# Kernel tuning notes

Measured on AMD Instinct MI355X. Metric: run time of the kernel, lower is better.

The kernel has to match this reference:

```python
import jax, jax.numpy as jnp
import numpy as np

B, S, D, T = 64, 128, 512, 64  # batch, encoder len, dim_model, longest_coor

def setup_inputs() -> dict:
    key = jax.random.key(0)
    ks = jax.random.split(key, 10)
    def rn(k, shape, s=0.02):
        return jax.random.normal(k, shape, dtype=jnp.float32) * s
    return dict(
        e_all=jax.random.normal(ks[0], (B, S, D), dtype=jnp.float32),
        e_last=jax.random.normal(ks[1], (1, B, D), dtype=jnp.float32),
        Wa_w=rn(ks[2], (D, D)), Wa_b=jnp.zeros((D,), jnp.float32),
        Ua_w=rn(ks[3], (D, D)), Ua_b=jnp.zeros((D,), jnp.float32),
        Va_w=rn(ks[4], (D, 1)), Va_b=jnp.zeros((1,), jnp.float32),
        W_ih=rn(ks[5], (3 * D, D + 3)),  # GRU input weights, input = cat(attn[D], coord[3])
        W_hh=rn(ks[6], (3 * D, D)),
        b_ih=jnp.zeros((3 * D,), jnp.float32),
        b_hh=jnp.zeros((3 * D,), jnp.float32),
        Wo_w=rn(ks[7], (D, 3)), Wo_b=jnp.zeros((3,), jnp.float32),
    )

def reference(e_all, e_last, Wa_w, Wa_b, Ua_w, Ua_b, Va_w, Va_b,
              W_ih, W_hh, b_ih, b_hh, Wo_w, Wo_b):
    # Ua(keys) is step-invariant: hoist out of the decode loop (same math).
    Uk = e_all @ Ua_w + Ua_b                      # [B,S,D]
    h0 = e_last[0]                                # [B,D]
    x0 = jnp.zeros((e_all.shape[0], 3), e_all.dtype)

    def step(carry, _):
        h, x = carry
        # Bahdanau attention: query = current hidden state
        q = h @ Wa_w + Wa_b                       # [B,D]
        scores = jnp.squeeze(jnp.tanh(q[:, None, :] + Uk) @ Va_w, -1) + Va_b  # [B,S]
        w = jax.nn.softmax(scores, axis=-1)       # [B,S]
        ctx = jnp.einsum('bs,bsd->bd', w, e_all)  # [B,D]
        # single-step GRU, input = cat(context, prev coord)
        gin = jnp.concatenate([ctx, x], axis=-1)  # [B,D+3]
        gi = gin @ W_ih.T + b_ih                  # [B,3D]
        gh = h @ W_hh.T + b_hh                    # [B,3D]
        gir, giz, gin_n = jnp.split(gi, 3, axis=-1)
        ghr, ghz, ghn = jnp.split(gh, 3, axis=-1)
        r = jax.nn.sigmoid(gir + ghr)
        z = jax.nn.sigmoid(giz + ghz)
        n = jnp.tanh(gin_n + r * ghn)
        h_new = (1.0 - z) * n + z * h             # [B,D]
        out = h_new @ Wo_w + Wo_b                 # [B,3]
        return (h_new, out), (out, w)

    (hT, _), (outs, attns) = jax.lax.scan(step, (h0, x0), None, length=T)
    d_outputs = jnp.transpose(outs, (1, 0, 2))    # [B,T,3]
    cross_attn = jnp.transpose(attns, (1, 0, 2))  # [B,T,S]
    return d_outputs, hT[None], cross_attn
```

## Files before the change

### kernel.cpp

```cpp
#include <hip/hip_runtime.h>

typedef unsigned int u32;
typedef unsigned long long u64;
typedef float f32x4 __attribute__((ext_vector_type(4)));
typedef short short8 __attribute__((ext_vector_type(8)));

#define OFF_UKB 0u
#define OFF_QX  16777216u
#define OFF_EX  17563648u
#define G_BYTES 73728u

#define OFF_OUT_HT  12288u
#define OFF_OUT_ATT 45056u

#define NBLK 192
#define NTHR 512
#define DYN_LDS 145408
#define PREP_LDS 36864

__device__ __forceinline__ float fast_rcp(float x) { return __builtin_amdgcn_rcpf(x); }
__device__ __forceinline__ float tanh5(float x) {
    float e = __expf(2.f * x);
    return 1.f - 2.f * fast_rcp(e + 1.f);
}
__device__ __forceinline__ float sigm_f(float x) { return fast_rcp(1.f + __expf(-x)); }

__device__ __forceinline__ u32 packbf2(float a, float b) {
    u32 ua = __float_as_uint(a); ua += 0x7FFFu + ((ua >> 16) & 1u);
    u32 ub = __float_as_uint(b); ub += 0x7FFFu + ((ub >> 16) & 1u);
    return (ua >> 16) | (ub & 0xFFFF0000u);
}
__device__ __forceinline__ float2 unpackbf2(u32 u) {
    return make_float2(__uint_as_float(u << 16), __uint_as_float(u & 0xFFFF0000u));
}
__device__ __forceinline__ float bf16hi(float x, float& lo) {
    u32 u = __float_as_uint(x); u += 0x7FFFu + ((u >> 16) & 1u); u &= 0xFFFF0000u;
    const float h = __uint_as_float(u); lo = x - h; return h;
}

__device__ __forceinline__ u64 cload64(const u64* p) {
    return __hip_atomic_load(p, __ATOMIC_RELAXED, __HIP_MEMORY_SCOPE_AGENT);
}
__device__ __forceinline__ void cstore64(u64* p, u64 v) {
    __hip_atomic_store(p, v, __ATOMIC_RELAXED, __HIP_MEMORY_SCOPE_AGENT);
}
__device__ __forceinline__ u32 cload32(const u32* p) {
    return __hip_atomic_load(p, __ATOMIC_RELAXED, __HIP_MEMORY_SCOPE_AGENT);
}
__device__ __forceinline__ void cstore32(u32* p, u32 v) {
    __hip_atomic_store(p, v, __ATOMIC_RELAXED, __HIP_MEMORY_SCOPE_AGENT);
}

union U8 { u32 u[4]; uint4 q; short8 s; };

__global__ __launch_bounds__(256) void prep_kernel(
    const float* __restrict__ e_all, const float* __restrict__ e_last,
    const float* __restrict__ Ua_w,  const float* __restrict__ Ua_b,
    float* __restrict__ ws)
{
    extern __shared__ char pls[];
    u32* Ahi = (u32*)pls;
    u32* Alo = Ahi + 64 * 36;
    u32* Bhi = Alo + 64 * 36;
    u32* Blo = Bhi + 64 * 36;

    u32* UKB = (u32*)((char*)ws + OFF_UKB);

    const int blk = blockIdx.x, tid = threadIdx.x;
    const int gtid = blk * 256 + tid, gstride = 1024 * 256;

    for (int i = gtid; i < 5120; i += gstride) {
        const int g = i / 1280, j = i - g * 1280;
        ((u32*)((char*)ws + OFF_EX + (size_t)g * G_BYTES + 65536))[j] = 0u;
    }
    for (int i = gtid; i < 65536; i += gstride)
        ((u64*)((char*)ws + OFF_QX))[i] = 0ull;
    for (int i = gtid; i < 8192; i += gstride) {
        const int g = i >> 11, i2 = i & 2047;
        const float* ep = e_last + ((size_t)(g * 16 + (i2 >> 7)) * 512) + 4 * (i2 & 127);
        u64* HX = (u64*)((char*)ws + OFF_EX + (size_t)g * G_BYTES);
        HX[i2] = (u64)packbf2(ep[0], ep[1]) | ((u64)packbf2(ep[2], ep[3]) << 32);
    }

    const int r0 = (blk >> 3) * 64, c0 = (blk & 7) * 64;
    const int lane = tid & 63, wv = tid >> 6;
    const int mn = lane & 15, quad = lane >> 4;

    f32x4 acc[4];
    #pragma unroll
    for (int rg = 0; rg < 4; ++rg) acc[rg] = (f32x4){0.f, 0.f, 0.f, 0.f};

    for (int ks = 0; ks < 8; ++ks) {
        if (ks) __syncthreads();
        for (int i = tid; i < 1024; i += 256) {
            const int row = i >> 4, q4i = i & 15;
            const float4 e = *(const float4*)(e_all + (size_t)(r0 + row) * 512 + ks * 64 + 4 * q4i);
            float l0, l1, l2, l3;
            const float h0 = bf16hi(e.x, l0), h1 = bf16hi(e.y, l1);
            const float h2 = bf16hi(e.z, l2), h3 = bf16hi(e.w, l3);
            Ahi[row * 36 + 2 * q4i]     = packbf2(h0, h1);
            Ahi[row * 36 + 2 * q4i + 1] = packbf2(h2, h3);
            Alo[row * 36 + 2 * q4i]     = packbf2(l0, l1);
            Alo[row * 36 + 2 * q4i + 1] = packbf2(l2, l3);
        }
        for (int i = tid; i < 2048; i += 256) {
            const int col = i & 63, kp = i >> 6;
            const float b0 = Ua_w[(size_t)(ks * 64 + 2 * kp) * 512 + c0 + col];
            const float b1 = Ua_w[(size_t)(ks * 64 + 2 * kp + 1) * 512 + c0 + col];
            float l0, l1;
            const float h0 = bf16hi(b0, l0), h1 = bf16hi(b1, l1);
            Bhi[col * 36 + kp] = packbf2(h0, h1);
            Blo[col * 36 + kp] = packbf2(l0, l1);
        }
        __syncthreads();
        #pragma unroll
        for (int kb = 0; kb < 2; ++kb) {
            const int fo = kb * 16 + quad * 4;
            U8 bh, bl;
            bh.q = *(const uint4*)(Bhi + (wv * 16 + mn) * 36 + fo);
            bl.q = *(const uint4*)(Blo + (wv * 16 + mn) * 36 + fo);
            #pragma unroll
            for (int rg = 0; rg < 4; ++rg) {
                U8 ah, al;
                ah.q = *(const uint4*)(Ahi + (rg * 16 + mn) * 36 + fo);
                al.q = *(const uint4*)(Alo + (rg * 16 + mn) * 36 + fo);
                acc[rg] = __builtin_amdgcn_mfma_f32_16x16x32_bf16(al.s, bh.s, acc[rg], 0, 0, 0);
                acc[rg] = __builtin_amdgcn_mfma_f32_16x16x32_bf16(ah.s, bl.s, acc[rg], 0, 0, 0);
                acc[rg] = __builtin_amdgcn_mfma_f32_16x16x32_bf16(ah.s, bh.s, acc[rg], 0, 0, 0);
            }
        }
    }
    const int col = c0 + wv * 16 + mn;
    const float bias = Ua_b[col];
    #pragma unroll
    for (int rg = 0; rg < 4; ++rg) {
        #pragma unroll
        for (int reg = 0; reg < 4; ++reg) {
            const float v = acc[rg][reg] + bias;
            const float v1 = __shfl_down(v, 1);
            if (!(mn & 1))
                UKB[(size_t)(r0 + rg * 16 + quad * 4 + reg) * 256 + (col >> 1)] = packbf2(v, v1);
        }
    }
}

__global__ __launch_bounds__(512, 1) void decode_kernel(
    const float* __restrict__ e_all,
    const float* __restrict__ e_last,
    const float* __restrict__ Wa_w,  const float* __restrict__ Wa_b,
    const float* __restrict__ Va_w,
    const float* __restrict__ W_ih,  const float* __restrict__ W_hh,
    const float* __restrict__ b_ih,  const float* __restrict__ b_hh,
    const float* __restrict__ Wo_w,  const float* __restrict__ Wo_b,
    float* __restrict__ out, float* __restrict__ ws)
{
    extern __shared__ char smraw[];

    const u32* UKB = (const u32*)((char*)ws + OFF_UKB);

    const int tid = threadIdx.x;
    const int bi  = blockIdx.x;
    const int g   = bi / 48, r = bi % 48;
    const int lane = tid & 63, wv = tid >> 6;

    char* gbase = (char*)ws + OFF_EX + (size_t)g * G_BYTES;
    u64* HX = (u64*)gbase;
    u64* CX = (u64*)(gbase + 32768);
    u32* FH = (u32*)(gbase + 65536);
    u32* FC = (u32*)(gbase + 67584);

    if (r < 16) {
        const int bl = r, b = g * 16 + bl;
        u32*   EuL  = (u32*)smraw;
        float* eq_s = (float*)(smraw + 131072);
        float* w_s  = (float*)(smraw + 133120);
        float* red  = (float*)(smraw + 133632);
        float* psq  = (float*)(smraw + 133696);

        const u64* QXR = (const u64*)((char*)ws + OFF_QX + (size_t)g * 131072u);

        {
            const uint4* src = (const uint4*)(UKB + (size_t)b * 32768);
            uint4* dst = (uint4*)EuL;
            #pragma unroll
            for (int i = 0; i < 16; ++i) {
                uint4 u = src[tid + 512 * i];
                float2 p;
                p = unpackbf2(u.x); u.x = packbf2(__expf(2.f * p.x), __expf(2.f * p.y));
                p = unpackbf2(u.y); u.y = packbf2(__expf(2.f * p.x), __expf(2.f * p.y));
                p = unpackbf2(u.z); u.z = packbf2(__expf(2.f * p.x), __expf(2.f * p.y));
                p = unpackbf2(u.w); u.w = packbf2(__expf(2.f * p.x), __expf(2.f * p.y));
                dst[tid + 512 * i] = u;
            }
        }
        uint2 ereg[32];
        {
            const int dq = tid & 127, sg = tid >> 7;
            const float* ep = e_all + (size_t)b * 65536;
            #pragma unroll
            for (int si = 0; si < 32; ++si) {
                const float4 e = *(const float4*)(ep + (size_t)(sg * 32 + si) * 512 + 4 * dq);
                ereg[si] = make_uint2(packbf2(e.x, e.y), packbf2(e.z, e.w));
            }
        }
        const int kl = lane & 15;
        float4 va2a[4], va2b[4];
        float vaSum = 0.f;
        #pragma unroll
        for (int it = 0; it < 4; ++it) {
            const float4 a  = *(const float4*)(Va_w + (it * 16 + kl) * 8);
            const float4 b2 = *(const float4*)(Va_w + (it * 16 + kl) * 8 + 4);
            vaSum += a.x + a.y + a.z + a.w + b2.x + b2.y + b2.z + b2.w;
            va2a[it] = make_float4(-2.f * a.x,  -2.f * a.y,  -2.f * a.z,  -2.f * a.w);
            va2b[it] = make_float4(-2.f * b2.x, -2.f * b2.y, -2.f * b2.z, -2.f * b2.w);
        }
        __syncthreads();

        for (int t = 0; t < 64; ++t) {
            const int slot = t & 1;
            const u32 tg = (u32)(t + 1);
            u64* CxS = CX + slot * 2048;
            const u64* QxS = QXR + slot * 8192 + (size_t)bl * 512;

            if (tid < 256) {
                u64 v0 = cload64(QxS + 2 * tid), v1 = cload64(QxS + 2 * tid + 1);
                while ((u32)(v0 >> 32) != tg) v0 = cload64(QxS + 2 * tid);
                while ((u32)(v1 >> 32) != tg) v1 = cload64(QxS + 2 * tid + 1);
                ((float2*)eq_s)[tid] = make_float2(__uint_as_float((u32)v0),
                                                   __uint_as_float((u32)v1));
            }
            __syncthreads();

            {
                float4 eqa[4], eqb[4];
                const float4* q4 = (const float4*)eq_s;
                #pragma unroll
                for (int it = 0; it < 4; ++it) {
                    eqa[it] = q4[(it * 16 + kl) * 2];  eqb[it] = q4[(it * 16 + kl) * 2 + 1];
                }
                const int sbase = wv * 16 + (lane >> 4);
                #pragma unroll
                for (int sg = 0; sg < 4; ++sg) {
                    const int s = sbase + sg * 4;
                    const uint4* uk4 = (const uint4*)EuL + (size_t)s * 64;
                    float acc = vaSum;
                    #pragma unroll
                    for (int it = 0; it < 4; ++it) {
                        const uint4 u = uk4[it * 16 + kl];
                        const float2 u0 = unpackbf2(u.x), u1 = unpackbf2(u.y);
                        const float2 u2 = unpackbf2(u.z), u3 = unpackbf2(u.w);
                        acc = fmaf(va2a[it].x, fast_rcp(fmaf(eqa[it].x, u0.x, 1.f)), acc);
                        acc = fmaf(va2a[it].y, fast_rcp(fmaf(eqa[it].y, u0.y, 1.f)), acc);
                        acc = fmaf(va2a[it].z, fast_rcp(fmaf(eqa[it].z, u1.x, 1.f)), acc);
                        acc = fmaf(va2a[it].w, fast_rcp(fmaf(eqa[it].w, u1.y, 1.f)), acc);
                        acc = fmaf(va2b[it].x, fast_rcp(fmaf(eqb[it].x, u2.x, 1.f)), acc);
                        acc = fmaf(va2b[it].y, fast_rcp(fmaf(eqb[it].y, u2.y, 1.f)), acc);
                        acc = fmaf(va2b[it].z, fast_rcp(fmaf(eqb[it].z, u3.x, 1.f)), acc);
                        acc = fmaf(va2b[it].w, fast_rcp(fmaf(eqb[it].w, u3.y, 1.f)), acc);
                    }
                    acc += __shfl_xor(acc, 1); acc += __shfl_xor(acc, 2);
                    acc += __shfl_xor(acc, 4); acc += __shfl_xor(acc, 8);
                    if (kl == 0) w_s[s] = __expf(acc);
                }
            }
            __syncthreads();

            if (tid < 64) {
                float sm = w_s[tid] + w_s[tid + 64];
                #pragma unroll
                for (int off = 32; off > 0; off >>= 1) sm += __shfl_down(sm, off);
                if (tid == 0) red[1] = fast_rcp(sm);
            }
            {
                const int dq = tid & 127, sg = tid >> 7;
                float4 a = {0.f, 0.f, 0.f, 0.f};
                #pragma unroll
                for (int si = 0; si < 32; ++si) {
                    const float wgt = w_s[sg * 32 + si];
                    const float2 e0 = unpackbf2(ereg[si].x), e1 = unpackbf2(ereg[si].y);
                    a.x = fmaf(wgt, e0.x, a.x);
                    a.y = fmaf(wgt, e0.y, a.y);
                    a.z = fmaf(wgt, e1.x, a.z);
                    a.w = fmaf(wgt, e1.y, a.w);
                }
                ((float4*)psq)[sg * 128 + dq] = a;
            }
            __syncthreads();
            if (tid < 128) {
                const float rn = red[1];
                const float4* p4 = (const float4*)psq;
                float4 a = p4[tid], b2 = p4[128 + tid], c2 = p4[256 + tid], d2 = p4[384 + tid];
                const float rx = (a.x + b2.x + c2.x + d2.x) * rn;
                const float ry = (a.y + b2.y + c2.y + d2.y) * rn;
                const float rz = (a.z + b2.z + c2.z + d2.z) * rn;
                const float rw = (a.w + b2.w + c2.w + d2.w) * rn;
                cstore64(CxS + bl * 128 + tid,
                         (u64)packbf2(rx, ry) | ((u64)packbf2(rz, rw) << 32));
            }
            __syncthreads();
            if (tid == 0) cstore32(FC + bl * 16, (u32)(t + 1));
            else if (tid >= 128 && tid < 256)
                out[OFF_OUT_ATT + ((size_t)b * 64 + t) * 128 + (tid - 128)] = w_s[tid - 128] * red[1];
        }
    } else {
        const int idx = r - 16, d0 = idx * 16;
        u32*   hbu  = (u32*)smraw;
        u32*   cbu  = (u32*)(smraw + 16640);
        float* gh_s = (float*)(smraw + 33280);
        float* gi_s = (float*)(smraw + 36352);
        float* x_s  = (float*)(smraw + 39424);
        float* wx_s = (float*)(smraw + 39616);
        float* wo_s = (float*)(smraw + 40192);

        u64* QXW = (u64*)((char*)ws + OFF_QX + (size_t)g * 131072u);

        const int mn = lane & 15, quad = lane >> 4;

        short8 bfrag[16];
        float qbias = 0.f;
        if (wv < 3) {
            const float* wrow = W_hh + (size_t)(wv * 512 + d0 + mn) * 512;
            #pragma unroll
            for (int kb = 0; kb < 16; ++kb) {
                const int k0 = kb * 32 + quad * 8;
                U8 tpk;
                #pragma unroll
                for (int c = 0; c < 4; ++c)
                    tpk.u[c] = packbf2(wrow[k0 + 2 * c], wrow[k0 + 2 * c + 1]);
                bfrag[kb] = tpk.s;
            }
        } else if (wv < 6) {
            const float* wrow = W_ih + (size_t)((wv - 3) * 512 + d0 + mn) * 515;
            #pragma unroll
            for (int kb = 0; kb < 16; ++kb) {
                const int k0 = kb * 32 + quad * 8;
                U8 tpk;
                #pragma unroll
                for (int c = 0; c < 4; ++c)
                    tpk.u[c] = packbf2(wrow[k0 + 2 * c], wrow[k0 + 2 * c + 1]);
                bfrag[kb] = tpk.s;
            }
        } else if (wv == 6) {
            #pragma unroll
            for (int kb = 0; kb < 16; ++kb) {
                const int k0 = kb * 32 + quad * 8;
                U8 tpk;
                #pragma unroll
                for (int c = 0; c < 4; ++c)
                    tpk.u[c] = packbf2(Wa_w[(size_t)(k0 + 2 * c) * 512 + d0 + mn],
                                       Wa_w[(size_t)(k0 + 2 * c + 1) * 512 + d0 + mn]);
                bfrag[kb] = tpk.s;
            }
            qbias = Wa_b[d0 + mn];
        }
        if (tid < 144) {
            const int dd = tid / 9, rem = tid - dd * 9, g3 = rem / 3, c = rem - g3 * 3;
            wx_s[tid] = W_ih[(size_t)(g3 * 512 + d0 + dd) * 515 + 512 + c];
        }
        for (int i = tid; i < 1536; i += 512) wo_s[i] = Wo_w[i];
        if (tid < 3) wo_s[1536 + tid] = Wo_b[tid];

        const int gb = tid >> 4, gd = tid & 15;
        float hold = 0.f, bih[3], bhh[3];
        if (tid < 256) {
            hold = e_last[(size_t)(g * 16 + gb) * 512 + d0 + gd];
            #pragma unroll
            for (int g3 = 0; g3 < 3; ++g3) {
                bih[g3] = b_ih[g3 * 512 + d0 + gd];
                bhh[g3] = b_hh[g3 * 512 + d0 + gd];
            }
        }

        for (int t = 0; t < 64; ++t) {
            const int slot = t & 1;
            const u64* HxS = HX + slot * 2048;
            const u64* CxS = CX + slot * 2048;
            u64* HxW = HX + ((t + 1) & 1) * 2048;

            if (lane < 16) {
                const u32* f = FH + ((wv & 1) * 16 + lane) * 16;
                while (cload32(f) < (u32)t) {}
            }
            #pragma unroll
            for (int u = 0; u < 4; ++u) {
                const int i = tid + 512 * u;
                const u64 v = cload64(HxS + i);
                *(u64*)(hbu + (i >> 7) * 260 + (i & 127) * 2) = v;
            }
            __syncthreads();

            if (wv < 3) {
                f32x4 c = {0.f, 0.f, 0.f, 0.f};
                #pragma unroll
                for (int kb = 0; kb < 16; ++kb) {
                    U8 a; a.q = *(const uint4*)(hbu + mn * 260 + kb * 16 + quad * 4);
                    c = __builtin_amdgcn_mfma_f32_16x16x32_bf16(a.s, bfrag[kb], c, 0, 0, 0);
                }
                #pragma unroll
                for (int reg = 0; reg < 4; ++reg)
                    gh_s[((quad * 4 + reg) * 16 + mn) * 3 + wv] = c[reg];
            } else if (wv < 6) {
                if (lane < 16) { const u32* f = FC + lane * 16; while (cload32(f) < (u32)(t + 1)) {} }
                const int thr = (wv - 3) * 64 + lane;
                for (int i = thr; i < 2048; i += 192) {
                    const u64 v = cload64(CxS + i);
                    *(u64*)(cbu + (i >> 7) * 260 + (i & 127) * 2) = v;
                }
            } else if (wv == 6) {
                f32x4 c = {0.f, 0.f, 0.f, 0.f};
                #pragma unroll
                for (int kb = 0; kb < 16; ++kb) {
                    U8 a; a.q = *(const uint4*)(hbu + mn * 260 + kb * 16 + quad * 4);
                    c = __builtin_amdgcn_mfma_f32_16x16x32_bf16(a.s, bfrag[kb], c, 0, 0, 0);
                }
                u64* QxW = QXW + slot * 8192;
                const u64 tg64 = (u64)(u32)(t + 1) << 32;
                #pragma unroll
                for (int reg = 0; reg < 4; ++reg) {
                    const float q0 = c[reg] + qbias;
                    const float e  = __expf(2.f * q0);
                    cstore64(QxW + (size_t)(quad * 4 + reg) * 512 + d0 + mn,
                             tg64 | (u64)__float_as_uint(e));
                }
            } else {
                const int tt = tid - 448, cb = tt >> 2, kl = tt & 3;
                if (t > 0) {
                    float a0 = 0.f, a1 = 0.f, a2 = 0.f;
                    #pragma unroll 4
                    for (int c = 0; c < 64; ++c) {
                        const int p = kl * 64 + c;
                        const float2 hv = unpackbf2(hbu[cb * 260 + p]);
                        const float* w0 = wo_s + 2 * p * 3;
                        a0 = fmaf(hv.x, w0[0], fmaf(hv.y, w0[3], a0));
                        a1 = fmaf(hv.x, w0[1], fmaf(hv.y, w0[4], a1));
                        a2 = fmaf(hv.x, w0[2], fmaf(hv.y, w0[5], a2));
                    }
                    a0 += __shfl_xor(a0, 1); a1 += __shfl_xor(a1, 1); a2 += __shfl_xor(a2, 1);
                    a0 += __shfl_xor(a0, 2); a1 += __shfl_xor(a1, 2); a2 += __shfl_xor(a2, 2);
                    if (kl == 0) {
                        x_s[cb * 3 + 0] = a0 + wo_s[1536];
                        x_s[cb * 3 + 1] = a1 + wo_s[1537];
                        x_s[cb * 3 + 2] = a2 + wo_s[1538];
                    }
                } else if (tt < 48) x_s[tt] = 0.f;
            }
            __syncthreads();

            if (wv >= 3 && wv < 6) {
                f32x4 c = {0.f, 0.f, 0.f, 0.f};
                #pragma unroll
                for (int kb = 0; kb < 16; ++kb) {
                    U8 a; a.q = *(const uint4*)(cbu + mn * 260 + kb * 16 + quad * 4);
                    c = __builtin_amdgcn_mfma_f32_16x16x32_bf16(a.s, bfrag[kb], c, 0, 0, 0);
                }
                #pragma unroll
                for (int reg = 0; reg < 4; ++reg)
                    gi_s[((quad * 4 + reg) * 16 + mn) * 3 + (wv - 3)] = c[reg];
            } else if (idx == 0 && t > 0 && tid < 48) {
                out[((size_t)(g * 16 + tid / 3) * 64 + (t - 1)) * 3 + tid % 3] = x_s[tid];
            }
            __syncthreads();

            if (tid < 256) {
                const int ob = (gb * 16 + gd) * 3;
                const float x0 = x_s[gb * 3 + 0], x1 = x_s[gb * 3 + 1], x2 = x_s[gb * 3 + 2];
                const float giR = gi_s[ob + 0] + bih[0]
                                + x0 * wx_s[gd * 9 + 0] + x1 * wx_s[gd * 9 + 1] + x2 * wx_s[gd * 9 + 2];
                const float giZ = gi_s[ob + 1] + bih[1]
                                + x0 * wx_s[gd * 9 + 3] + x1 * wx_s[gd * 9 + 4] + x2 * wx_s[gd * 9 + 5];
                const float giN = gi_s[ob + 2] + bih[2]
                                + x0 * wx_s[gd * 9 + 6] + x1 * wx_s[gd * 9 + 7] + x2 * wx_s[gd * 9 + 8];
                const float ghR = gh_s[ob + 0] + bhh[0];
                const float ghZ = gh_s[ob + 1] + bhh[1];
                const float ghN = gh_s[ob + 2] + bhh[2];
                const float rg = sigm_f(giR + ghR);
                const float zg = sigm_f(giZ + ghZ);
                const float ng = tanh5(giN + rg * ghN);
                const float hnew = (1.f - zg) * ng + zg * hold;
                hold = hnew;
                const float s1 = __shfl_down(hnew, 1);
                const float s2 = __shfl_down(hnew, 2);
                const float s3 = __shfl_down(hnew, 3);
                if ((gd & 3) == 0)
                    cstore64(HxW + gb * 128 + ((d0 + gd) >> 2),
                             (u64)packbf2(hnew, s1) | ((u64)packbf2(s2, s3) << 32));
                if (t == 63)
                    out[OFF_OUT_HT + (size_t)(g * 16 + gb) * 512 + d0 + gd] = hnew;
            }
            __syncthreads();
            if (tid == 0) cstore32(FH + idx * 16, (u32)(t + 1));
        }

        if (tid < 32) { const u32* f = FH + tid * 16; while (cload32(f) < 64u) {} }
        __syncthreads();
        #pragma unroll
        for (int u = 0; u < 4; ++u) {
            const int i = tid + 512 * u;
            const u64 v = cload64(HX + i);
            *(u64*)(hbu + (i >> 7) * 260 + (i & 127) * 2) = v;
        }
        __syncthreads();
        if (wv >= 6) {
            const int tt = tid - 384, cb = tt >> 3, kl = tt & 7;
            float a0 = 0.f, a1 = 0.f, a2 = 0.f;
            #pragma unroll 4
            for (int c = 0; c < 32; ++c) {
                const int p = kl * 32 + c;
                const float2 hv = unpackbf2(hbu[cb * 260 + p]);
                const float* w0 = wo_s + 2 * p * 3;
                a0 = fmaf(hv.x, w0[0], fmaf(hv.y, w0[3], a0));
                a1 = fmaf(hv.x, w0[1], fmaf(hv.y, w0[4], a1));
                a2 = fmaf(hv.x, w0[2], fmaf(hv.y, w0[5], a2));
            }
            a0 += __shfl_xor(a0, 1); a1 += __shfl_xor(a1, 1); a2 += __shfl_xor(a2, 1);
            a0 += __shfl_xor(a0, 2); a1 += __shfl_xor(a1, 2); a2 += __shfl_xor(a2, 2);
            a0 += __shfl_xor(a0, 4); a1 += __shfl_xor(a1, 4); a2 += __shfl_xor(a2, 4);
            if (kl == 0) {
                x_s[cb * 3 + 0] = a0 + wo_s[1536];
                x_s[cb * 3 + 1] = a1 + wo_s[1537];
                x_s[cb * 3 + 2] = a2 + wo_s[1538];
            }
        }
        __syncthreads();
        if (idx == 0 && tid < 48)
            out[((size_t)(g * 16 + tid / 3) * 64 + 63) * 3 + tid % 3] = x_s[tid];
    }
}

extern "C" void kernel_launch(void* const* d_in, const int* in_sizes, int n_in,
                              void* d_out, int out_size, void* d_ws, size_t ws_size,
                              hipStream_t stream) {
    const float* e_all  = (const float*)d_in[0];
    const float* e_last = (const float*)d_in[1];
    const float* Wa_w   = (const float*)d_in[2];
    const float* Wa_b   = (const float*)d_in[3];
    const float* Ua_w   = (const float*)d_in[4];
    const float* Ua_b   = (const float*)d_in[5];
    const float* Va_w   = (const float*)d_in[6];
    const float* W_ih   = (const float*)d_in[8];
    const float* W_hh   = (const float*)d_in[9];
    const float* b_ih   = (const float*)d_in[10];
    const float* b_hh   = (const float*)d_in[11];
    const float* Wo_w   = (const float*)d_in[12];
    const float* Wo_b   = (const float*)d_in[13];
    float* outp = (float*)d_out;
    float* ws   = (float*)d_ws;

    hipFuncSetAttribute((const void*)prep_kernel,
                        hipFuncAttributeMaxDynamicSharedMemorySize, PREP_LDS);
    hipFuncSetAttribute((const void*)decode_kernel,
                        hipFuncAttributeMaxDynamicSharedMemorySize, DYN_LDS);

    hipLaunchKernelGGL(prep_kernel, dim3(1024), dim3(256), PREP_LDS, stream,
                       e_all, e_last, Ua_w, Ua_b, ws);

    void* args[] = { (void*)&e_all, (void*)&e_last, (void*)&Wa_w, (void*)&Wa_b,
                     (void*)&Va_w,
                     (void*)&W_ih, (void*)&W_hh, (void*)&b_ih, (void*)&b_hh,
                     (void*)&Wo_w, (void*)&Wo_b, (void*)&outp, (void*)&ws };
    hipError_t err = hipLaunchCooperativeKernel((void*)decode_kernel, dim3(NBLK), dim3(NTHR),
                                                args, DYN_LDS, stream);
    if (err != hipSuccess) {
        hipLaunchKernelGGL(decode_kernel, dim3(NBLK), dim3(NTHR), DYN_LDS, stream,
                           e_all, e_last, Wa_w, Wa_b, Va_w,
                           W_ih, W_hh, b_ih, b_hh, Wo_w, Wo_b, outp, ws);
    }
}
```

Baseline: 914.1 us.

## Replace context flag handshake with per-element tagged stores and polling

Attention blocks now write each packed bf16 context pair together with a step tag in the upper 32 bits. The separate __syncthreads and per-batch flag store are removed. GRU blocks poll the tagged words directly, using four waves (including the q-producer wave) that each keep 16 outstanding loads, instead of spinning on a flag and then copying. This removes a barrier and a flag round-trip from the inter-block critical path, at the cost of twice the context traffic and a larger workspace.

```diff
diff --git a/kernel.cpp b/kernel.cpp
--- a/kernel.cpp
+++ b/kernel.cpp
@@ -8,7 +8,7 @@
 #define OFF_UKB 0u
 #define OFF_QX  16777216u
 #define OFF_EX  17563648u
-#define G_BYTES 73728u
+#define G_BYTES 102400u
 
 #define OFF_OUT_HT  12288u
 #define OFF_OUT_ATT 45056u
@@ -69,9 +69,13 @@
     const int blk = blockIdx.x, tid = threadIdx.x;
     const int gtid = blk * 256 + tid, gstride = 1024 * 256;
 
-    for (int i = gtid; i < 5120; i += gstride) {
-        const int g = i / 1280, j = i - g * 1280;
-        ((u32*)((char*)ws + OFF_EX + (size_t)g * G_BYTES + 65536))[j] = 0u;
+    for (int i = gtid; i < 2048; i += gstride) {
+        const int g = i >> 9, j = i & 511;
+        ((u32*)((char*)ws + OFF_EX + (size_t)g * G_BYTES + 98304))[j] = 0u;
+    }
+    for (int i = gtid; i < 32768; i += gstride) {
+        const int g = i >> 13, j = i & 8191;
+        ((u64*)((char*)ws + OFF_EX + (size_t)g * G_BYTES + 32768))[j] = 0ull;
     }
     for (int i = gtid; i < 65536; i += gstride)
         ((u64*)((char*)ws + OFF_QX))[i] = 0ull;
@@ -166,8 +170,7 @@
     char* gbase = (char*)ws + OFF_EX + (size_t)g * G_BYTES;
     u64* HX = (u64*)gbase;
     u64* CX = (u64*)(gbase + 32768);
-    u32* FH = (u32*)(gbase + 65536);
-    u32* FC = (u32*)(gbase + 67584);
+    u32* FH = (u32*)(gbase + 98304);
 
     if (r < 16) {
         const int bl = r, b = g * 16 + bl;
@@ -219,7 +222,7 @@
         for (int t = 0; t < 64; ++t) {
             const int slot = t & 1;
             const u32 tg = (u32)(t + 1);
-            u64* CxS = CX + slot * 2048;
+            u64* CxS = CX + slot * 4096;
             const u64* QxS = QXR + slot * 8192 + (size_t)bl * 512;
 
             if (tid < 256) {
@@ -294,13 +297,12 @@
                 const float ry = (a.y + b2.y + c2.y + d2.y) * rn;
                 const float rz = (a.z + b2.z + c2.z + d2.z) * rn;
                 const float rw = (a.w + b2.w + c2.w + d2.w) * rn;
-                cstore64(CxS + bl * 128 + tid,
-                         (u64)packbf2(rx, ry) | ((u64)packbf2(rz, rw) << 32));
-            }
-            __syncthreads();
-            if (tid == 0) cstore32(FC + bl * 16, (u32)(t + 1));
-            else if (tid >= 128 && tid < 256)
+                const u64 tg64 = (u64)tg << 32;
+                cstore64(CxS + (size_t)bl * 256 + 2 * tid,     tg64 | (u64)packbf2(rx, ry));
+                cstore64(CxS + (size_t)bl * 256 + 2 * tid + 1, tg64 | (u64)packbf2(rz, rw));
+            } else if (tid < 256) {
                 out[OFF_OUT_ATT + ((size_t)b * 64 + t) * 128 + (tid - 128)] = w_s[tid - 128] * red[1];
+            }
         }
     } else {
         const int idx = r - 16, d0 = idx * 16;
@@ -373,8 +375,9 @@
 
         for (int t = 0; t < 64; ++t) {
             const int slot = t & 1;
+            const u32 tg = (u32)(t + 1);
             const u64* HxS = HX + slot * 2048;
-            const u64* CxS = CX + slot * 2048;
+            const u64* CxS = CX + slot * 4096;
             u64* HxW = HX + ((t + 1) & 1) * 2048;
 
             if (lane < 16) {
@@ -399,30 +402,7 @@
                 #pragma unroll
                 for (int reg = 0; reg < 4; ++reg)
                     gh_s[((quad * 4 + reg) * 16 + mn) * 3 + wv] = c[reg];
-            } else if (wv < 6) {
-                if (lane < 16) { const u32* f = FC + lane * 16; while (cload32(f) < (u32)(t + 1)) {} }
-                const int thr = (wv - 3) * 64 + lane;
-                for (int i = thr; i < 2048; i += 192) {
-                    const u64 v = cload64(CxS + i);
-                    *(u64*)(cbu + (i >> 7) * 260 + (i & 127) * 2) = v;
-                }
-            } else if (wv == 6) {
-                f32x4 c = {0.f, 0.f, 0.f, 0.f};
-                #pragma unroll
-                for (int kb = 0; kb < 16; ++kb) {
-                    U8 a; a.q = *(const uint4*)(hbu + mn * 260 + kb * 16 + quad * 4);
-                    c = __builtin_amdgcn_mfma_f32_16x16x32_bf16(a.s, bfrag[kb], c, 0, 0, 0);
-                }
-                u64* QxW = QXW + slot * 8192;
-                const u64 tg64 = (u64)(u32)(t + 1) << 32;
-                #pragma unroll
-                for (int reg = 0; reg < 4; ++reg) {
-                    const float q0 = c[reg] + qbias;
-                    const float e  = __expf(2.f * q0);
-                    cstore64(QxW + (size_t)(quad * 4 + reg) * 512 + d0 + mn,
-                             tg64 | (u64)__float_as_uint(e));
-                }
-            } else {
+            } else if (wv == 7) {
                 const int tt = tid - 448, cb = tt >> 2, kl = tt & 3;
                 if (t > 0) {
                     float a0 = 0.f, a1 = 0.f, a2 = 0.f;
@@ -443,6 +423,42 @@
                         x_s[cb * 3 + 2] = a2 + wo_s[1538];
                     }
                 } else if (tt < 48) x_s[tt] = 0.f;
+            } else {
+                if (wv == 6) {
+                    f32x4 c = {0.f, 0.f, 0.f, 0.f};
+                    #pragma unroll
+                    for (int kb = 0; kb < 16; ++kb) {
+                        U8 a; a.q = *(const uint4*)(hbu + mn * 260 + kb * 16 + quad * 4);
+                        c = __builtin_amdgcn_mfma_f32_16x16x32_bf16(a.s, bfrag[kb], c, 0, 0, 0);
+                    }
+                    u64* QxW = QXW + slot * 8192;
+                    const u64 tg64 = (u64)tg << 32;
+                    #pragma unroll
+                    for (int reg = 0; reg < 4; ++reg) {
+                        const float q0 = c[reg] + qbias;
+                        const float e  = __expf(2.f * q0);
+                        cstore64(QxW + (size_t)(quad * 4 + reg) * 512 + d0 + mn,
+                                 tg64 | (u64)__float_as_uint(e));
+                    }
+                }
+                const int thr = (wv - 3) * 64 + lane;
+                u64 cc[16];
+                u32 pend = 0xFFFFu;
+                #pragma unroll
+                for (int k = 0; k < 16; ++k) cc[k] = cload64(CxS + thr + 256 * k);
+                #pragma unroll
+                for (int k = 0; k < 16; ++k)
+                    if ((u32)(cc[k] >> 32) == tg) { cbu[k * 260 + thr] = (u32)cc[k]; pend &= ~(1u << k); }
+                while (pend) {
+                    #pragma unroll
+                    for (int k = 0; k < 16; ++k)
+                        if (pend & (1u << k)) cc[k] = cload64(CxS + thr + 256 * k);
+                    #pragma unroll
+                    for (int k = 0; k < 16; ++k)
+                        if ((pend & (1u << k)) && (u32)(cc[k] >> 32) == tg) {
+                            cbu[k * 260 + thr] = (u32)cc[k]; pend &= ~(1u << k);
+                        }
+                }
             }
             __syncthreads();
 
```

New measurement: 839.1 us. -8.2%, faster.
